# Kernel tuning notes

Hardware: AMD Instinct MI355X
Metric: run time of the kernel (lower is better)

## Reference

```python
import jax, jax.numpy as jnp
import numpy as np

DEPTH = 6
HEADS = 8
DIM = 512
DH = DIM // HEADS          # 64
SEQ = 512
BATCH = 8
MEM = 4096                 # KNN memory slots per batch element (scaled from 64000)
TOPK = 32                  # num_retrieved_memories
KNN_LAYERS = (3, 4)        # memorizing_layers=(4,5), 1-indexed -> 0-indexed 3,4
FF = 4 * DIM


def setup_inputs() -> dict:
    key = jax.random.key(0)
    ks = jax.random.split(key, 18)
    s = 0.02
    return {
        "x":     jax.random.normal(ks[0], (BATCH, SEQ, DIM), jnp.float32),
        "Wq":    jax.random.normal(ks[1], (DEPTH, DIM, DIM), jnp.float32) * s,
        "Wk":    jax.random.normal(ks[2], (DEPTH, DIM, DIM), jnp.float32) * s,
        "Wv":    jax.random.normal(ks[3], (DEPTH, DIM, DIM), jnp.float32) * s,
        "Wo":    jax.random.normal(ks[4], (DEPTH, DIM, DIM), jnp.float32) * s,
        "ln1_s": jnp.ones((DEPTH, DIM), jnp.float32),
        "ln1_b": jnp.zeros((DEPTH, DIM), jnp.float32),
        "ln2_s": jnp.ones((DEPTH, DIM), jnp.float32),
        "ln2_b": jnp.zeros((DEPTH, DIM), jnp.float32),
        "W1":    jax.random.normal(ks[5], (DEPTH, DIM, FF), jnp.float32) * s,
        "W2":    jax.random.normal(ks[6], (DEPTH, FF, DIM), jnp.float32) * s,
        "lnf_s": jnp.ones((DIM,), jnp.float32),
        "lnf_b": jnp.zeros((DIM,), jnp.float32),
        # pre-populated KNN memory banks (keys/values in head dim), one per memorizing layer
        "mem_k": jax.random.normal(ks[7], (len(KNN_LAYERS), BATCH, MEM, DH), jnp.float32),
        "mem_v": jax.random.normal(ks[8], (len(KNN_LAYERS), BATCH, MEM, DH), jnp.float32),
    }


def _ln(x, s, b):
    m = x.mean(-1, keepdims=True)
    v = ((x - m) ** 2).mean(-1, keepdims=True)
    return (x - m) * jax.lax.rsqrt(v + 1e-5) * s + b


def _gather_mem(mem, idx):
    # mem: (b, M, d), idx: (b, h, n, K) -> (b, h, n, K, d)
    return jax.vmap(lambda m, i: m[i])(mem, idx)


def reference(x, Wq, Wk, Wv, Wo, ln1_s, ln1_b, ln2_s, ln2_b, W1, W2,
              lnf_s, lnf_b, mem_k, mem_v):
    b, n, d = x.shape
    scale = DH ** -0.5
    causal = jnp.tril(jnp.ones((n, n), dtype=bool))
    neg = jnp.float32(-1e9)
    mem_i = 0
    for l in range(DEPTH):
        h = _ln(x, ln1_s[l], ln1_b[l])
        q = (h @ Wq[l]).reshape(b, n, HEADS, DH)
        k = (h @ Wk[l]).reshape(b, n, HEADS, DH)
        v = (h @ Wv[l]).reshape(b, n, HEADS, DH)
        sim = jnp.einsum('bihd,bjhd->bhij', q, k) * scale
        sim = jnp.where(causal, sim, neg)
        if l in KNN_LAYERS:
            mk, mv = mem_k[mem_i], mem_v[mem_i]              # (b, M, dh)
            # KNN search: dense scoring + top-k retrieval
            sim_all = jnp.einsum('bihd,bmd->bhim', q, mk) * scale  # (b,h,n,M)
            top_sim, top_idx = jax.lax.top_k(sim_all, TOPK)        # (b,h,n,K)
            gv = _gather_mem(mv, top_idx)                          # (b,h,n,K,dh)
            # joint softmax over [retrieved memories, local causal]
            logits = jnp.concatenate([top_sim, sim], axis=-1)
            attn = jax.nn.softmax(logits, axis=-1)
            a_mem, a_loc = attn[..., :TOPK], attn[..., TOPK:]
            out = (jnp.einsum('bhik,bhikd->bhid', a_mem, gv)
                   + jnp.einsum('bhij,bjhd->bhid', a_loc, v))
            mem_i += 1
        else:
            attn = jax.nn.softmax(sim, axis=-1)
            out = jnp.einsum('bhij,bjhd->bhid', attn, v)
        out = out.transpose(0, 2, 1, 3).reshape(b, n, d) @ Wo[l]
        x = x + out
        h2 = _ln(x, ln2_s[l], ln2_b[l])
        x = x + jax.nn.gelu(h2 @ W1[l]) @ W2[l]
    return _ln(x, lnf_s, lnf_b)
```

## Files before the change

kernel.cpp:

```cpp
#include <hip/hip_runtime.h>
#include <math.h>

#define BB 8
#define NN 512
#define DD 512
#define HH 8
#define DHH 64
#define FFF 2048
#define MEMM 4096
#define TOPKK 32
#define DEPTHH 6
#define NT (BB*NN)
#define QKVS 1536

typedef __bf16 bf16x8 __attribute__((ext_vector_type(8)));
typedef __bf16 bf16x4 __attribute__((ext_vector_type(4)));
typedef float f32x4 __attribute__((ext_vector_type(4)));

template <int OBF16>
__global__ __launch_bounds__(256) void ln_kernel(const float* __restrict__ xin,
                                                 const float* __restrict__ g,
                                                 const float* __restrict__ bt,
                                                 void* __restrict__ outv) {
  __shared__ float red[4];
  int tok = blockIdx.x;
  const float* xr = xin + (size_t)tok * DD;
  int t = threadIdx.x;
  float v0 = xr[t], v1 = xr[t + 256];
  float s = v0 + v1;
#pragma unroll
  for (int m = 32; m; m >>= 1) s += __shfl_xor(s, m, 64);
  if ((t & 63) == 0) red[t >> 6] = s;
  __syncthreads();
  float mean = (red[0] + red[1] + red[2] + red[3]) * (1.0f / 512.0f);
  float d0 = v0 - mean, d1 = v1 - mean;
  float vv = d0 * d0 + d1 * d1;
#pragma unroll
  for (int m = 32; m; m >>= 1) vv += __shfl_xor(vv, m, 64);
  __syncthreads();
  if ((t & 63) == 0) red[t >> 6] = vv;
  __syncthreads();
  float var = (red[0] + red[1] + red[2] + red[3]) * (1.0f / 512.0f);
  float inv = rsqrtf(var + 1e-5f);
  float o0 = d0 * inv * g[t] + bt[t];
  float o1 = d1 * inv * g[t + 256] + bt[t + 256];
  if (OBF16) {
    __bf16* out = (__bf16*)outv;
    out[(size_t)tok * DD + t] = (__bf16)o0;
    out[(size_t)tok * DD + t + 256] = (__bf16)o1;
  } else {
    float* out = (float*)outv;
    out[(size_t)tok * DD + t] = o0;
    out[(size_t)tok * DD + t + 256] = o1;
  }
}

__device__ inline float gelu_f(float x) {
  float x3 = x * x * x;
  return 0.5f * x * (1.0f + tanhf(0.7978845608028654f * (x + 0.044715f * x3)));
}

__global__ __launch_bounds__(256) void transpose_all_kernel(
    const float* __restrict__ Wq, const float* __restrict__ Wk,
    const float* __restrict__ Wv, const float* __restrict__ Wo,
    const float* __restrict__ W1, const float* __restrict__ W2,
    __bf16* __restrict__ wqT, __bf16* __restrict__ wkT,
    __bf16* __restrict__ wvT, __bf16* __restrict__ woT,
    __bf16* __restrict__ w1T, __bf16* __restrict__ w2T) {
  __shared__ float tile[32][33];
  int tid = blockIdx.x;
  const float* src; __bf16* dst; int K, N, tt;
  if (tid < 1024) {
    int which = tid >> 8; tt = tid & 255; K = 512; N = 512;
    src = (which == 0) ? Wq : (which == 1) ? Wk : (which == 2) ? Wv : Wo;
    dst = (which == 0) ? wqT : (which == 1) ? wkT : (which == 2) ? wvT : woT;
  } else if (tid < 2048) {
    tt = tid - 1024; K = 512; N = 2048; src = W1; dst = w1T;
  } else {
    tt = tid - 2048; K = 2048; N = 512; src = W2; dst = w2T;
  }
  int nx = N >> 5;
  int n0 = (tt % nx) * 32, k0 = (tt / nx) * 32;
  int tx = threadIdx.x & 31, ty = threadIdx.x >> 5;
#pragma unroll
  for (int i = 0; i < 4; i++) {
    int r = ty + i * 8;
    tile[r][tx] = src[(size_t)(k0 + r) * N + n0 + tx];
  }
  __syncthreads();
#pragma unroll
  for (int i = 0; i < 4; i++) {
    int r = ty + i * 8;
    dst[(size_t)(n0 + r) * K + k0 + tx] = (__bf16)tile[tx][r];
  }
}

__device__ __forceinline__ void gload16(const __bf16* g, __bf16* lds) {
  __builtin_amdgcn_global_load_lds(
      (const __attribute__((address_space(1))) void*)g,
      (__attribute__((address_space(3))) void*)lds, 16, 0, 0);
}

template <int EPI, int OBF16>
__global__ __launch_bounds__(256) void gemm_mfma128(const __bf16* __restrict__ A,
                                                    const __bf16* __restrict__ Bt,
                                                    const float* __restrict__ R,
                                                    void* __restrict__ Cout,
                                                    int M, int N, int K) {
  __shared__ __align__(16) __bf16 Als[128 * 64];
  __shared__ __align__(16) __bf16 Bls[128 * 64];
  int t = threadIdx.x;
  int bn = blockIdx.x, bm = blockIdx.y;
  int lane = t & 63, w = t >> 6;
  int wr = w >> 1, wc = w & 1;
  int m15 = lane & 15, q = lane >> 4;
  f32x4 acc[4][4] = {};
  for (int kt = 0; kt < K; kt += 64) {
    __syncthreads();
#pragma unroll
    for (int i = 0; i < 4; i++) {
      int rg = w * 32 + i * 8;
      int row = rg + (lane >> 3);
      int lcol = (lane & 7) * 8;
      gload16(A + (size_t)(bm * 128 + row) * K + kt + lcol, &Als[rg * 64]);
      gload16(Bt + (size_t)(bn * 128 + row) * K + kt + lcol, &Bls[rg * 64]);
    }
    __syncthreads();
#pragma unroll
    for (int ks = 0; ks < 2; ks++) {
      bf16x8 af[4], bfr[4];
#pragma unroll
      for (int mt = 0; mt < 4; mt++)
        af[mt] = *(const bf16x8*)&Als[(wr * 64 + mt * 16 + m15) * 64 + (ks * 4 + q) * 8];
#pragma unroll
      for (int nt = 0; nt < 4; nt++)
        bfr[nt] = *(const bf16x8*)&Bls[(wc * 64 + nt * 16 + m15) * 64 + (ks * 4 + q) * 8];
#pragma unroll
      for (int mt = 0; mt < 4; mt++)
#pragma unroll
        for (int nt = 0; nt < 4; nt++)
          acc[mt][nt] = __builtin_amdgcn_mfma_f32_16x16x32_bf16(af[mt], bfr[nt],
                                                                acc[mt][nt], 0, 0, 0);
    }
  }
#pragma unroll
  for (int mt = 0; mt < 4; mt++) {
#pragma unroll
    for (int nt = 0; nt < 4; nt++) {
      int gc = bn * 128 + wc * 64 + nt * 16 + m15;
#pragma unroll
      for (int r = 0; r < 4; r++) {
        int gr = bm * 128 + wr * 64 + mt * 16 + q * 4 + r;
        size_t off = (size_t)gr * N + gc;
        float v = acc[mt][nt][r];
        if (EPI == 1) v = gelu_f(v);
        if (EPI == 2) v += R[off];
        if (OBF16) ((__bf16*)Cout)[off] = (__bf16)v;
        else       ((float*)Cout)[off] = v;
      }
    }
  }
}

template <int EPI, int OBF16>
__global__ __launch_bounds__(256) void gemm_mfma64(const __bf16* __restrict__ A,
                                                   const __bf16* __restrict__ Bt,
                                                   const float* __restrict__ R,
                                                   void* __restrict__ Cout,
                                                   int M, int N, int K) {
  __shared__ __align__(16) __bf16 Als[128 * 64];
  __shared__ __align__(16) __bf16 Bls[64 * 64];
  int t = threadIdx.x;
  int bn = blockIdx.x, bm = blockIdx.y;
  int lane = t & 63, w = t >> 6;
  int wr = w >> 1, wc = w & 1;
  int m15 = lane & 15, q = lane >> 4;
  f32x4 acc[4][2] = {};
  for (int kt = 0; kt < K; kt += 64) {
    __syncthreads();
#pragma unroll
    for (int i = 0; i < 4; i++) {
      int rg = w * 32 + i * 8;
      int row = rg + (lane >> 3);
      int lcol = (lane & 7) * 8;
      gload16(A + (size_t)(bm * 128 + row) * K + kt + lcol, &Als[rg * 64]);
    }
#pragma unroll
    for (int i = 0; i < 2; i++) {
      int rg = w * 16 + i * 8;
      int row = rg + (lane >> 3);
      int lcol = (lane & 7) * 8;
      gload16(Bt + (size_t)(bn * 64 + row) * K + kt + lcol, &Bls[rg * 64]);
    }
    __syncthreads();
#pragma unroll
    for (int ks = 0; ks < 2; ks++) {
      bf16x8 af[4], bfr[2];
#pragma unroll
      for (int mt = 0; mt < 4; mt++)
        af[mt] = *(const bf16x8*)&Als[(wr * 64 + mt * 16 + m15) * 64 + (ks * 4 + q) * 8];
#pragma unroll
      for (int nt = 0; nt < 2; nt++)
        bfr[nt] = *(const bf16x8*)&Bls[(wc * 32 + nt * 16 + m15) * 64 + (ks * 4 + q) * 8];
#pragma unroll
      for (int mt = 0; mt < 4; mt++)
#pragma unroll
        for (int nt = 0; nt < 2; nt++)
          acc[mt][nt] = __builtin_amdgcn_mfma_f32_16x16x32_bf16(af[mt], bfr[nt],
                                                                acc[mt][nt], 0, 0, 0);
    }
  }
#pragma unroll
  for (int mt = 0; mt < 4; mt++) {
#pragma unroll
    for (int nt = 0; nt < 2; nt++) {
      int gc = bn * 64 + wc * 32 + nt * 16 + m15;
#pragma unroll
      for (int r = 0; r < 4; r++) {
        int gr = bm * 128 + wr * 64 + mt * 16 + q * 4 + r;
        size_t off = (size_t)gr * N + gc;
        float v = acc[mt][nt][r];
        if (EPI == 1) v = gelu_f(v);
        if (EPI == 2) v += R[off];
        if (OBF16) ((__bf16*)Cout)[off] = (__bf16)v;
        else       ((float*)Cout)[off] = v;
      }
    }
  }
}

__global__ __launch_bounds__(256) void split_bf16_kernel(const float* __restrict__ src,
                                                         __bf16* __restrict__ hi,
                                                         __bf16* __restrict__ lo) {
  int i = blockIdx.x * 256 + threadIdx.x;
  float4 v = ((const float4*)src)[i];
  float xs[4] = {v.x, v.y, v.z, v.w};
  bf16x4 hv, lv;
#pragma unroll
  for (int e = 0; e < 4; e++) {
    __bf16 h = (__bf16)xs[e];
    hv[e] = h;
    lv[e] = (__bf16)(xs[e] - (float)h);
  }
  *(bf16x4*)&hi[(size_t)i * 4] = hv;
  *(bf16x4*)&lo[(size_t)i * 4] = lv;
}

__global__ __launch_bounds__(256) void vtrans_split_kernel(const float* __restrict__ qkv,
                                                           __bf16* __restrict__ vth,
                                                           __bf16* __restrict__ vtl) {
  __shared__ float tile[64 * 68];
  int tt = blockIdx.x, h = blockIdx.y, b = blockIdx.z;
  int t = threadIdx.x;
#pragma unroll
  for (int i = 0; i < 4; i++) {
    int lin = i * 256 + t, row = lin >> 4, c = (lin & 15) * 4;
    float4 x = *(const float4*)(qkv + ((size_t)(b * NN) + tt * 64 + row) * QKVS + 1024 + h * DHH + c);
    *(float4*)&tile[row * 68 + c] = x;
  }
  __syncthreads();
  int d = t >> 2, tb = (t & 3) * 16;
  float xs[16];
#pragma unroll
  for (int j = 0; j < 16; j++) xs[j] = tile[(tb + j) * 68 + d];
  bf16x8 h0, h1, l0, l1;
#pragma unroll
  for (int j = 0; j < 8; j++) {
    __bf16 a = (__bf16)xs[j];
    h0[j] = a; l0[j] = (__bf16)(xs[j] - (float)a);
    __bf16 bmv = (__bf16)xs[8 + j];
    h1[j] = bmv; l1[j] = (__bf16)(xs[8 + j] - (float)bmv);
  }
  size_t ob = ((size_t)(b * HH + h) * 64 + d) * NN + tt * 64 + tb;
  *(bf16x8*)(vth + ob) = h0; *(bf16x8*)(vth + ob + 8) = h1;
  *(bf16x8*)(vtl + ob) = l0; *(bf16x8*)(vtl + ob + 8) = l1;
}

__global__ __launch_bounds__(256) void knn_score_mfma(const float* __restrict__ q,
                                                      const __bf16* __restrict__ khi,
                                                      const __bf16* __restrict__ klo,
                                                      float* __restrict__ S,
                                                      int bh0) {
  __shared__ __bf16 Kls[2][128 * 72];
  int it = blockIdx.x, bh = bh0 + blockIdx.y;
  int b = bh >> 3, h = bh & 7;
  int t = threadIdx.x;
  int lane = t & 63, w = t >> 6;
  int m15 = lane & 15, kg = lane >> 4;
  const float scale = 0.125f;

  bf16x8 aqh[2][2], aql[2][2];
#pragma unroll
  for (int rf = 0; rf < 2; rf++)
#pragma unroll
    for (int ks = 0; ks < 2; ks++) {
      const float* qp = q + ((size_t)(b * NN) + it * 32 + rf * 16 + m15) * QKVS +
                        h * DHH + ks * 32 + kg * 8;
      float4 x0 = *(const float4*)qp;
      float4 x1 = *(const float4*)(qp + 4);
      float xs[8] = {x0.x, x0.y, x0.z, x0.w, x1.x, x1.y, x1.z, x1.w};
#pragma unroll
      for (int e = 0; e < 8; e++) {
        __bf16 hv = (__bf16)xs[e];
        aqh[rf][ks][e] = hv;
        aql[rf][ks][e] = (__bf16)(xs[e] - (float)hv);
      }
    }

  const __bf16* khb = khi + (size_t)b * MEMM * DHH;
  const __bf16* klb = klo + (size_t)b * MEMM * DHH;
  size_t srow0 = (size_t)blockIdx.y * NN + it * 32;

  for (int mt = 0; mt < MEMM; mt += 128) {
    __syncthreads();
#pragma unroll
    for (int i = 0; i < 4; i++) {
      int lin = i * 256 + t;
      int row = lin >> 3, cb = (lin & 7) * 8;
      *(uint4*)&Kls[0][row * 72 + cb] = *(const uint4*)(khb + (size_t)(mt + row) * DHH + cb);
      *(uint4*)&Kls[1][row * 72 + cb] = *(const uint4*)(klb + (size_t)(mt + row) * DHH + cb);
    }
    __syncthreads();
    f32x4 acc[2][2] = {};
#pragma unroll
    for (int ks = 0; ks < 2; ks++) {
      bf16x8 bh2[2], bl2[2];
#pragma unroll
      for (int cf = 0; cf < 2; cf++) {
        int row = w * 32 + cf * 16 + m15;
        bh2[cf] = *(const bf16x8*)&Kls[0][row * 72 + ks * 32 + kg * 8];
        bl2[cf] = *(const bf16x8*)&Kls[1][row * 72 + ks * 32 + kg * 8];
      }
#pragma unroll
      for (int rf = 0; rf < 2; rf++)
#pragma unroll
        for (int cf = 0; cf < 2; cf++) {
          acc[rf][cf] = __builtin_amdgcn_mfma_f32_16x16x32_bf16(aqh[rf][ks], bh2[cf], acc[rf][cf], 0, 0, 0);
          acc[rf][cf] = __builtin_amdgcn_mfma_f32_16x16x32_bf16(aql[rf][ks], bh2[cf], acc[rf][cf], 0, 0, 0);
          acc[rf][cf] = __builtin_amdgcn_mfma_f32_16x16x32_bf16(aqh[rf][ks], bl2[cf], acc[rf][cf], 0, 0, 0);
        }
    }
#pragma unroll
    for (int rf = 0; rf < 2; rf++)
#pragma unroll
      for (int cf = 0; cf < 2; cf++) {
        int col = mt + w * 32 + cf * 16 + m15;
#pragma unroll
        for (int rr = 0; rr < 4; rr++)
          S[(srow0 + rf * 16 + kg * 4 + rr) * MEMM + col] = acc[rf][cf][rr] * scale;
      }
  }
}

__global__ __launch_bounds__(256, 4) void knn_select_kernel(const float* __restrict__ S,
                                                            float* __restrict__ topv,
                                                            int* __restrict__ topi,
                                                            int row_base) {
  int lane = threadIdx.x & 63;
  int row = blockIdx.x * 4 + (threadIdx.x >> 6);
  const float* srow = S + (size_t)row * MEMM;
  unsigned u[64];
#pragma unroll
  for (int i = 0; i < 64; i++) {
    union { float f; unsigned b; } cv;
    cv.f = srow[i * 64 + lane];
    unsigned b = cv.b;
    u[i] = (b & 0x80000000u) ? ~b : (b | 0x80000000u);
  }
  unsigned T = 0;
#pragma unroll 1
  for (int bit = 31; bit >= 0; --bit) {
    unsigned Tp = T | (1u << bit);
    int c = 0;
#pragma unroll
    for (int i = 0; i < 64; i++) c += (u[i] >= Tp) ? 1 : 0;
#pragma unroll
    for (int m = 32; m; m >>= 1) c += __shfl_xor(c, m, 64);
    if (c >= TOPKK) {
      T = Tp;
      if (c == TOPKK) break;
    }
  }
  unsigned long long below = (1ull << lane) - 1ull;
  float* tvrow = topv + (size_t)(row_base + row) * TOPKK;
  int* tirow = topi + (size_t)(row_base + row) * TOPKK;
  int g = 0;
#pragma unroll
  for (int i = 0; i < 64; i++) {
    bool f = u[i] > T;
    unsigned long long m = __ballot(f);
    if (f) {
      int pos = g + __popcll(m & below);
      union { unsigned b; float f2; } rv;
      rv.b = (u[i] & 0x80000000u) ? (u[i] & 0x7fffffffu) : ~u[i];
      tvrow[pos] = rv.f2;
      tirow[pos] = i * 64 + lane;
    }
    g += __popcll(m);
  }
#pragma unroll
  for (int i = 0; i < 64; i++) {
    if (g < TOPKK) {
      bool f = (u[i] == T);
      unsigned long long m = __ballot(f);
      if (f) {
        int pos = g + __popcll(m & below);
        if (pos < TOPKK) {
          union { unsigned b; float f2; } rv;
          rv.b = (T & 0x80000000u) ? (T & 0x7fffffffu) : ~T;
          tvrow[pos] = rv.f2;
          tirow[pos] = i * 64 + lane;
        }
      }
      g += __popcll(m);
    }
  }
}

__device__ __forceinline__ void insert32vi(float (&rtv)[32], int (&rti)[32],
                                           float sv, int idx, float& thr) {
  float mv = rtv[0], mv2 = INFINITY;
  int mi = 0;
#pragma unroll
  for (int k = 1; k < 32; k++) {
    float v = rtv[k];
    bool lt = v < mv;
    mv2 = lt ? mv : fminf(mv2, v);
    mv = lt ? v : mv;
    mi = lt ? k : mi;
  }
#pragma unroll
  for (int k = 0; k < 32; k++) {
    bool hit = (k == mi);
    rtv[k] = hit ? sv : rtv[k];
    rti[k] = hit ? idx : rti[k];
  }
  thr = fminf(mv2, sv);
}

__global__ __launch_bounds__(256) void knn_mfma_topk(const float* __restrict__ q,
                                                     const __bf16* __restrict__ khi,
                                                     const __bf16* __restrict__ klo,
                                                     float* __restrict__ topv,
                                                     int* __restrict__ topi) {
  __shared__ __bf16 Kls[2][128 * 72];
  __shared__ float scb[32][132];
  __shared__ unsigned short midx[32 * 260];
  __shared__ float rthr[8][32];
  int it = blockIdx.x, h = blockIdx.y, b = blockIdx.z;
  int t = threadIdx.x;
  int lane = t & 63, w = t >> 6;
  int m15 = lane & 15, kg = lane >> 4;
  const float scale = 0.125f;
  bf16x8 aqh[2][2], aql[2][2];
#pragma unroll
  for (int rf = 0; rf < 2; rf++)
#pragma unroll
    for (int ks = 0; ks < 2; ks++) {
      const float* qp = q + ((size_t)(b * NN) + it * 32 + rf * 16 + m15) * QKVS +
                        h * DHH + ks * 32 + kg * 8;
      float4 x0 = *(const float4*)qp;
      float4 x1 = *(const float4*)(qp + 4);
      float xs[8] = {x0.x, x0.y, x0.z, x0.w, x1.x, x1.y, x1.z, x1.w};
#pragma unroll
      for (int e = 0; e < 8; e++) {
        __bf16 hv = (__bf16)xs[e];
        aqh[rf][ks][e] = hv;
        aql[rf][ks][e] = (__bf16)(xs[e] - (float)hv);
      }
    }
  int r = t & 31, p = t >> 5;
  rthr[p][r] = -INFINITY;
  float rtv[32]; int rti[32];
#pragma unroll
  for (int k = 0; k < 32; k++) { rtv[k] = -INFINITY; rti[k] = 0; }
  float thr = -INFINITY;
  const __bf16* khb = khi + (size_t)b * MEMM * DHH;
  const __bf16* klb = klo + (size_t)b * MEMM * DHH;

  for (int mt = 0; mt < MEMM; mt += 128) {
    __syncthreads();
#pragma unroll
    for (int i = 0; i < 4; i++) {
      int lin = i * 256 + t;
      int row = lin >> 3, cb = (lin & 7) * 8;
      *(uint4*)&Kls[0][row * 72 + cb] = *(const uint4*)(khb + (size_t)(mt + row) * DHH + cb);
      *(uint4*)&Kls[1][row * 72 + cb] = *(const uint4*)(klb + (size_t)(mt + row) * DHH + cb);
    }
    __syncthreads();
    f32x4 acc[2][2] = {};
#pragma unroll
    for (int ks = 0; ks < 2; ks++) {
      bf16x8 bh2[2], bl2[2];
#pragma unroll
      for (int cf = 0; cf < 2; cf++) {
        int row = w * 32 + cf * 16 + m15;
        bh2[cf] = *(const bf16x8*)&Kls[0][row * 72 + ks * 32 + kg * 8];
        bl2[cf] = *(const bf16x8*)&Kls[1][row * 72 + ks * 32 + kg * 8];
      }
#pragma unroll
      for (int rf = 0; rf < 2; rf++)
#pragma unroll
        for (int cf = 0; cf < 2; cf++) {
          acc[rf][cf] = __builtin_amdgcn_mfma_f32_16x16x32_bf16(aqh[rf][ks], bh2[cf], acc[rf][cf], 0, 0, 0);
          acc[rf][cf] = __builtin_amdgcn_mfma_f32_16x16x32_bf16(aql[rf][ks], bh2[cf], acc[rf][cf], 0, 0, 0);
          acc[rf][cf] = __builtin_amdgcn_mfma_f32_16x16x32_bf16(aqh[rf][ks], bl2[cf], acc[rf][cf], 0, 0, 0);
        }
    }
#pragma unroll
    for (int rf = 0; rf < 2; rf++)
#pragma unroll
      for (int cf = 0; cf < 2; cf++) {
        int col = w * 32 + cf * 16 + m15;
#pragma unroll
        for (int rr = 0; rr < 4; rr++)
          scb[rf * 16 + kg * 4 + rr][col] = acc[rf][cf][rr] * scale;
      }
    __syncthreads();
    {
      float B2 = rthr[0][r];
#pragma unroll
      for (int j = 1; j < 8; j++) B2 = fmaxf(B2, rthr[j][r]);
      const float* srow = &scb[r][16 * p];
#pragma unroll 1
      for (int c = 0; c < 16; c++) {
        int cc = (c + r) & 15;
        float sv = srow[cc];
        if (sv > fmaxf(thr, B2))
          insert32vi(rtv, rti, sv, mt + 16 * p + cc, thr);
      }
      rthr[p][r] = thr;
    }
  }
  __syncthreads();
  float* mvals = (float*)&Kls[0][0];
#pragma unroll
  for (int k = 0; k < 32; k++) {
    int cc = (k + r) & 31;
    mvals[(size_t)260 * r + 32 * p + cc] = rtv[k];
    midx[(size_t)260 * r + 32 * p + cc] = (unsigned short)rti[k];
  }
  __syncthreads();
  if (t < 32) {
#pragma unroll 1
    for (int c = 0; c < 224; c++) {
      int cc = c + r; if (cc >= 224) cc -= 224;
      float sv = mvals[(size_t)260 * r + 32 + cc];
      if (sv > thr)
        insert32vi(rtv, rti, sv, (int)midx[(size_t)260 * r + 32 + cc], thr);
    }
    size_t rowg = ((size_t)b * HH + h) * NN + it * 32 + r;
#pragma unroll
    for (int k = 0; k < 32; k++) {
      topv[rowg * TOPKK + k] = rtv[k];
      topi[rowg * TOPKK + k] = rti[k];
    }
  }
}

__global__ __launch_bounds__(256) void attn_mfma_kernel(
    const float* __restrict__ qkv,
    const __bf16* __restrict__ vth, const __bf16* __restrict__ vtl,
    __bf16* __restrict__ ao, const float* __restrict__ topv,
    const int* __restrict__ topi, const float* __restrict__ mem_v, int knn) {
  __shared__ __align__(16) __bf16 smem[27648];
  __bf16* Kh = smem;
  __bf16* Kl = smem + 4608;
  __bf16* Vh = smem + 9216;
  __bf16* Vl = smem + 13824;
  __bf16* Pw = smem + 18432;

  int flat = blockIdx.x;
  int bi = flat >> 6;
  int hb = flat & 63;
  int h = hb & 7, b = hb >> 3;
  int t = threadIdx.x, lane = t & 63, w = t >> 6;
  int q15 = lane & 15, g = lane >> 4;
  const float scale = 0.125f;

  bf16x8 qh[2], ql[2];
  {
    const float* qp = qkv + ((size_t)(b * NN) + bi * 64 + w * 16 + q15) * QKVS + h * DHH;
#pragma unroll
    for (int ks = 0; ks < 2; ks++) {
      float4 x0 = *(const float4*)(qp + ks * 32 + g * 8);
      float4 x1 = *(const float4*)(qp + ks * 32 + g * 8 + 4);
      float xs[8] = {x0.x, x0.y, x0.z, x0.w, x1.x, x1.y, x1.z, x1.w};
#pragma unroll
      for (int e = 0; e < 8; e++) {
        __bf16 hv = (__bf16)xs[e];
        qh[ks][e] = hv;
        ql[ks][e] = (__bf16)(xs[e] - (float)hv);
      }
    }
  }
  int tr = t >> 4, kc = (t & 15) * 4;
  int td = t >> 3, tb = (t & 7) * 8;
  float4 kp0, kp1, kp2, kp3;
  uint4 vhp0, vhp1, vlp0, vlp1;

#define LOAD_TILE(jt_) do {                                                        \
    const float* kb_ = qkv + ((size_t)(b * NN) + (jt_) * 64 + tr) * QKVS + 512 +   \
                       h * DHH + kc;                                               \
    kp0 = *(const float4*)kb_;                                                     \
    kp1 = *(const float4*)(kb_ + (size_t)16 * QKVS);                               \
    kp2 = *(const float4*)(kb_ + (size_t)32 * QKVS);                               \
    kp3 = *(const float4*)(kb_ + (size_t)48 * QKVS);                               \
    size_t vb_ = ((size_t)(b * HH + h) * 64 + td) * NN + (jt_) * 64 + tb;          \
    vhp0 = *(const uint4*)(vth + vb_);                                             \
    vhp1 = *(const uint4*)(vth + vb_ + (size_t)32 * NN);                           \
    vlp0 = *(const uint4*)(vtl + vb_);                                             \
    vlp1 = *(const uint4*)(vtl + vb_ + (size_t)32 * NN);                           \
  } while (0)

#define STORE_K(kp_, ro_) do {                                                     \
    bf16x4 hv_, lv_;                                                               \
    float e0_ = kp_.x, e1_ = kp_.y, e2_ = kp_.z, e3_ = kp_.w;                      \
    hv_[0] = (__bf16)e0_; lv_[0] = (__bf16)(e0_ - (float)hv_[0]);                  \
    hv_[1] = (__bf16)e1_; lv_[1] = (__bf16)(e1_ - (float)hv_[1]);                  \
    hv_[2] = (__bf16)e2_; lv_[2] = (__bf16)(e2_ - (float)hv_[2]);                  \
    hv_[3] = (__bf16)e3_; lv_[3] = (__bf16)(e3_ - (float)hv_[3]);                  \
    *(bf16x4*)&Kh[((ro_) + tr) * 72 + kc] = hv_;                                   \
    *(bf16x4*)&Kl[((ro_) + tr) * 72 + kc] = lv_;                                   \
  } while (0)

  float m_run = -INFINITY, l_run = 0.f;
  f32x4 opv[4] = {};
  int ntiles = bi + 1;
  LOAD_TILE(0);
  for (int jt = 0; jt < ntiles; jt++) {
    __syncthreads();
    STORE_K(kp0, 0); STORE_K(kp1, 16); STORE_K(kp2, 32); STORE_K(kp3, 48);
    *(uint4*)&Vh[td * 72 + tb] = vhp0;
    *(uint4*)&Vh[(32 + td) * 72 + tb] = vhp1;
    *(uint4*)&Vl[td * 72 + tb] = vlp0;
    *(uint4*)&Vl[(32 + td) * 72 + tb] = vlp1;
    if (jt + 1 < ntiles) LOAD_TILE(jt + 1);
    __syncthreads();
    int smax = (jt == bi) ? w : 3;
    float sc16[16];
    float tmax = -INFINITY;
#pragma unroll
    for (int s = 0; s < 4; s++) {
      if (s <= smax) {
        f32x4 accs = {};
#pragma unroll
        for (int ks = 0; ks < 2; ks++) {
          bf16x8 ah = *(const bf16x8*)&Kh[(s * 16 + q15) * 72 + ks * 32 + g * 8];
          bf16x8 al = *(const bf16x8*)&Kl[(s * 16 + q15) * 72 + ks * 32 + g * 8];
          accs = __builtin_amdgcn_mfma_f32_16x16x32_bf16(ah, qh[ks], accs, 0, 0, 0);
          accs = __builtin_amdgcn_mfma_f32_16x16x32_bf16(al, qh[ks], accs, 0, 0, 0);
          accs = __builtin_amdgcn_mfma_f32_16x16x32_bf16(ah, ql[ks], accs, 0, 0, 0);
        }
#pragma unroll
        for (int r = 0; r < 4; r++) {
          float sv = accs[r] * scale;
          if (jt == bi) {
            int kvg = jt * 64 + s * 16 + g * 4 + r;
            int qg = bi * 64 + w * 16 + q15;
            if (kvg > qg) sv = -INFINITY;
          }
          sc16[s * 4 + r] = sv;
          tmax = fmaxf(tmax, sv);
        }
      } else {
#pragma unroll
        for (int r = 0; r < 4; r++) sc16[s * 4 + r] = -INFINITY;
      }
    }
    tmax = fmaxf(tmax, __shfl_xor(tmax, 16, 64));
    tmax = fmaxf(tmax, __shfl_xor(tmax, 32, 64));
    float m_new = fmaxf(m_run, tmax);
    float psum = 0.f;
    __bf16 ph[16], pl[16];
#pragma unroll
    for (int i = 0; i < 16; i++) {
      float p = __expf(sc16[i] - m_new);
      psum += p;
      __bf16 hp = (__bf16)p;
      ph[i] = hp; pl[i] = (__bf16)(p - (float)hp);
    }
    psum += __shfl_xor(psum, 16, 64);
    psum += __shfl_xor(psum, 32, 64);
    float alpha = __expf(m_run - m_new);
    l_run = l_run * alpha + psum;
    m_run = m_new;
    __bf16* Ph = Pw + (w * 2 + 0) * 1152;
    __bf16* Pl = Pw + (w * 2 + 1) * 1152;
#pragma unroll
    for (int s = 0; s < 4; s++) {
      bf16x4 hv, lv;
#pragma unroll
      for (int r = 0; r < 4; r++) { hv[r] = ph[s * 4 + r]; lv[r] = pl[s * 4 + r]; }
      *(bf16x4*)&Ph[q15 * 72 + s * 16 + g * 4] = hv;
      *(bf16x4*)&Pl[q15 * 72 + s * 16 + g * 4] = lv;
    }
    __builtin_amdgcn_wave_barrier();
    float a0 = __shfl(alpha, g * 4 + 0, 64);
    float a1 = __shfl(alpha, g * 4 + 1, 64);
    float a2 = __shfl(alpha, g * 4 + 2, 64);
    float a3 = __shfl(alpha, g * 4 + 3, 64);
#pragma unroll
    for (int dsub = 0; dsub < 4; dsub++) {
      opv[dsub][0] *= a0; opv[dsub][1] *= a1;
      opv[dsub][2] *= a2; opv[dsub][3] *= a3;
    }
#pragma unroll
    for (int ks2 = 0; ks2 < 2; ks2++) {
      bf16x8 pah = *(const bf16x8*)&Ph[q15 * 72 + ks2 * 32 + g * 8];
      bf16x8 pal = *(const bf16x8*)&Pl[q15 * 72 + ks2 * 32 + g * 8];
#pragma unroll
      for (int dsub = 0; dsub < 4; dsub++) {
        bf16x8 vbh = *(const bf16x8*)&Vh[(dsub * 16 + q15) * 72 + ks2 * 32 + g * 8];
        bf16x8 vbl = *(const bf16x8*)&Vl[(dsub * 16 + q15) * 72 + ks2 * 32 + g * 8];
        opv[dsub] = __builtin_amdgcn_mfma_f32_16x16x32_bf16(pah, vbh, opv[dsub], 0, 0, 0);
        opv[dsub] = __builtin_amdgcn_mfma_f32_16x16x32_bf16(pal, vbh, opv[dsub], 0, 0, 0);
        opv[dsub] = __builtin_amdgcn_mfma_f32_16x16x32_bf16(pah, vbl, opv[dsub], 0, 0, 0);
      }
    }
  }
#undef LOAD_TILE
#undef STORE_K
  __syncthreads();
  float* scf  = (float*)smem;
  float* marr = (float*)(smem + 8704);
  float* larr = marr + 64;
  float* aarr = marr + 128;
  float* sc2  = (float*)(smem + 9216);
  int*   pidx = (int*)(smem + 13824);
#pragma unroll
  for (int dsub = 0; dsub < 4; dsub++)
#pragma unroll
    for (int r = 0; r < 4; r++)
      scf[(w * 16 + g * 4 + r) * 68 + dsub * 16 + q15] = opv[dsub][r];
  if (g == 0) { marr[w * 16 + q15] = m_run; larr[w * 16 + q15] = l_run; }
  __syncthreads();
  int r_ = t & 63, w4 = t >> 6;
  float acc16[16];
  if (knn) {
    size_t rowbase = ((size_t)b * HH + h) * NN + bi * 64;
    for (int rr = w * 16; rr < w * 16 + 16; rr++) {
      float s = (lane < TOPKK) ? topv[(rowbase + rr) * TOPKK + lane] : -INFINITY;
      float m_old = marr[rr];
      float tm = s;
#pragma unroll
      for (int m = 32; m; m >>= 1) tm = fmaxf(tm, __shfl_xor(tm, m, 64));
      float m_new = fmaxf(m_old, tm);
      float p = __expf(s - m_new);
      float ts = p;
#pragma unroll
      for (int m = 32; m; m >>= 1) ts += __shfl_xor(ts, m, 64);
      float alpha = __expf(m_old - m_new);
      if (lane < TOPKK) {
        sc2[rr * 33 + lane] = p;
        pidx[rr * 32 + lane] = topi[(rowbase + rr) * TOPKK + lane];
      }
      if (lane == 0) {
        marr[rr] = m_new; larr[rr] = larr[rr] * alpha + ts; aarr[rr] = alpha;
      }
    }
    __syncthreads();
    float al = aarr[r_];
#pragma unroll
    for (int dd = 0; dd < 16; dd++) acc16[dd] = scf[r_ * 68 + w4 * 16 + dd] * al;
    const float* mvb = mem_v + (size_t)b * MEMM * DHH;
#pragma unroll 1
    for (int kk = 0; kk < TOPKK; kk++) {
      float p = sc2[r_ * 33 + kk];
      const float* mrow = mvb + (size_t)pidx[r_ * 32 + kk] * DHH + w4 * 16;
#pragma unroll
      for (int dd = 0; dd < 16; dd += 4) {
        float4 m4 = *(const float4*)(mrow + dd);
        acc16[dd] += p * m4.x; acc16[dd + 1] += p * m4.y;
        acc16[dd + 2] += p * m4.z; acc16[dd + 3] += p * m4.w;
      }
    }
  } else {
#pragma unroll
    for (int dd = 0; dd < 16; dd++) acc16[dd] = scf[r_ * 68 + w4 * 16 + dd];
  }
  float linv = 1.f / larr[r_];
  bf16x8 o0, o1;
#pragma unroll
  for (int j = 0; j < 8; j++) {
    o0[j] = (__bf16)(acc16[j] * linv);
    o1[j] = (__bf16)(acc16[8 + j] * linv);
  }
  __bf16* aop = ao + ((size_t)(b * NN) + bi * 64 + r_) * DD + h * DHH + w4 * 16;
  *(bf16x8*)aop = o0;
  *(bf16x8*)(aop + 8) = o1;
}

extern "C" void kernel_launch(void* const* d_in, const int* in_sizes, int n_in,
                              void* d_out, int out_size, void* d_ws, size_t ws_size,
                              hipStream_t stream) {
  const float* x_in  = (const float*)d_in[0];
  const float* Wq    = (const float*)d_in[1];
  const float* Wk    = (const float*)d_in[2];
  const float* Wv    = (const float*)d_in[3];
  const float* Wo    = (const float*)d_in[4];
  const float* ln1_s = (const float*)d_in[5];
  const float* ln1_b = (const float*)d_in[6];
  const float* ln2_s = (const float*)d_in[7];
  const float* ln2_b = (const float*)d_in[8];
  const float* W1    = (const float*)d_in[9];
  const float* W2    = (const float*)d_in[10];
  const float* lnf_s = (const float*)d_in[11];
  const float* lnf_b = (const float*)d_in[12];
  const float* mem_k = (const float*)d_in[13];
  const float* mem_v = (const float*)d_in[14];

  float* ws  = (float*)d_ws;
  float*  xb    = ws;
  float*  qkvb  = ws + 2097152;
  __bf16* hb16  = (__bf16*)(ws + 8388608);
  __bf16* ao16  = (__bf16*)(ws + 9437184);
  __bf16* wqT   = (__bf16*)(ws + 10485760);
  __bf16* woT   = (__bf16*)(ws + 10878976);
  __bf16* w1T   = (__bf16*)(ws + 11010048);
  __bf16* w2T   = (__bf16*)(ws + 11534336);
  float*  tvb   = ws + 12058624;
  int*    tib   = (int*)(ws + 13107200);
  __bf16* ffb16 = (__bf16*)(ws + 2097152);
  __bf16* wkT   = wqT + 262144;
  __bf16* wvT   = wqT + 524288;
  __bf16* khi16 = (__bf16*)(ws + 8388608);
  __bf16* klo16 = (__bf16*)(ws + 9437184);

  const size_t base_floats = 14155776;
  const size_t slice_floats = (size_t)NN * MEMM;
  const size_t ws_floats = ws_size / sizeof(float);
  int nbh = 0;
  for (int c = 16; c >= 1; c >>= 1) {
    if (base_floats + (size_t)c * slice_floats <= ws_floats) { nbh = c; break; }
  }
  float* Sb = ws + base_floats;
  __bf16* vth = (__bf16*)(ws + base_floats);
  __bf16* vtl = (__bf16*)(ws + base_floats + 1048576);

  dim3 blk(256);
  const size_t DD2 = (size_t)DD * DD;
  for (int l = 0; l < DEPTHH; l++) {
    const float* xcur = (l == 0) ? x_in : xb;
    transpose_all_kernel<<<dim3(3072), blk, 0, stream>>>(
        Wq + l * DD2, Wk + l * DD2, Wv + l * DD2, Wo + l * DD2,
        W1 + (size_t)l * DD * FFF, W2 + (size_t)l * FFF * DD,
        wqT, wkT, wvT, woT, w1T, w2T);

    ln_kernel<1><<<NT, blk, 0, stream>>>(xcur, ln1_s + l * DD, ln1_b + l * DD, hb16);
    gemm_mfma64<0, 0><<<dim3(24, 32), blk, 0, stream>>>(hb16, wqT, nullptr, qkvb, NT, QKVS, DD);
    int mi = (l == 3) ? 0 : ((l == 4) ? 1 : -1);
    if (mi >= 0) {
      const float* mk = mem_k + (size_t)mi * BB * MEMM * DHH;
      split_bf16_kernel<<<dim3(BB * MEMM * DHH / 1024), blk, 0, stream>>>(mk, khi16, klo16);
      if (nbh > 0) {
        for (int bh0 = 0; bh0 < BB * HH; bh0 += nbh) {
          knn_score_mfma<<<dim3(16, nbh), blk, 0, stream>>>(qkvb, khi16, klo16, Sb, bh0);
          knn_select_kernel<<<dim3(nbh * NN / 4), blk, 0, stream>>>(Sb, tvb, tib, bh0 * NN);
        }
      } else {
        knn_mfma_topk<<<dim3(16, 8, 8), blk, 0, stream>>>(qkvb, khi16, klo16, tvb, tib);
      }
    }
    vtrans_split_kernel<<<dim3(8, 8, 8), blk, 0, stream>>>(qkvb, vth, vtl);
    attn_mfma_kernel<<<dim3(512), blk, 0, stream>>>(
        qkvb, vth, vtl, ao16, tvb, tib,
        mem_v + (size_t)(mi < 0 ? 0 : mi) * BB * MEMM * DHH, mi >= 0 ? 1 : 0);
    gemm_mfma64<2, 0><<<dim3(8, 32), blk, 0, stream>>>(ao16, woT, xcur, xb, NT, DD, DD);
    ln_kernel<1><<<NT, blk, 0, stream>>>(xb, ln2_s + l * DD, ln2_b + l * DD, hb16);
    gemm_mfma128<1, 1><<<dim3(16, 32), blk, 0, stream>>>(hb16, w1T, nullptr, ffb16, NT, FFF, DD);
    gemm_mfma64<2, 0><<<dim3(8, 32), blk, 0, stream>>>(ffb16, w2T, xb, xb, NT, DD, FFF);
  }
  ln_kernel<0><<<NT, blk, 0, stream>>>(xb, lnf_s, lnf_b, (float*)d_out);
}
```

Baseline: 1.910 ms.

## Enlarge KNN score tile, vectorize top-k select loads, allow larger score batches

The KNN scoring kernel now computes 64 query rows per block instead of 32, so each K tile staged in LDS is reused by twice as many MFMAs, and the grid shrinks to 8 row-tiles. The select kernel loads scores as uint4 per lane rather than strided scalars, and remaps output indices to match the new element order. The tie-fill loop now exits early once 32 entries are found. The host may also batch up to 64 (b,h) pairs per score/select launch when the workspace allows, which cuts launch count but needs more scratch and raises register pressure in the score kernel.

```diff
diff --git a/kernel.cpp b/kernel.cpp
--- a/kernel.cpp
+++ b/kernel.cpp
@@ -289,12 +289,12 @@
   int m15 = lane & 15, kg = lane >> 4;
   const float scale = 0.125f;
 
-  bf16x8 aqh[2][2], aql[2][2];
-#pragma unroll
-  for (int rf = 0; rf < 2; rf++)
+  bf16x8 aqh[4][2], aql[4][2];
+#pragma unroll
+  for (int rf = 0; rf < 4; rf++)
 #pragma unroll
     for (int ks = 0; ks < 2; ks++) {
-      const float* qp = q + ((size_t)(b * NN) + it * 32 + rf * 16 + m15) * QKVS +
+      const float* qp = q + ((size_t)(b * NN) + it * 64 + rf * 16 + m15) * QKVS +
                         h * DHH + ks * 32 + kg * 8;
       float4 x0 = *(const float4*)qp;
       float4 x1 = *(const float4*)(qp + 4);
@@ -309,7 +309,7 @@
 
   const __bf16* khb = khi + (size_t)b * MEMM * DHH;
   const __bf16* klb = klo + (size_t)b * MEMM * DHH;
-  size_t srow0 = (size_t)blockIdx.y * NN + it * 32;
+  size_t srow0 = (size_t)blockIdx.y * NN + it * 64;
 
   for (int mt = 0; mt < MEMM; mt += 128) {
     __syncthreads();
@@ -321,7 +321,7 @@
       *(uint4*)&Kls[1][row * 72 + cb] = *(const uint4*)(klb + (size_t)(mt + row) * DHH + cb);
     }
     __syncthreads();
-    f32x4 acc[2][2] = {};
+    f32x4 acc[4][2] = {};
 #pragma unroll
     for (int ks = 0; ks < 2; ks++) {
       bf16x8 bh2[2], bl2[2];
@@ -332,7 +332,7 @@
         bl2[cf] = *(const bf16x8*)&Kls[1][row * 72 + ks * 32 + kg * 8];
       }
 #pragma unroll
-      for (int rf = 0; rf < 2; rf++)
+      for (int rf = 0; rf < 4; rf++)
 #pragma unroll
         for (int cf = 0; cf < 2; cf++) {
           acc[rf][cf] = __builtin_amdgcn_mfma_f32_16x16x32_bf16(aqh[rf][ks], bh2[cf], acc[rf][cf], 0, 0, 0);
@@ -341,7 +341,7 @@
         }
     }
 #pragma unroll
-    for (int rf = 0; rf < 2; rf++)
+    for (int rf = 0; rf < 4; rf++)
 #pragma unroll
       for (int cf = 0; cf < 2; cf++) {
         int col = mt + w * 32 + cf * 16 + m15;
@@ -361,11 +361,14 @@
   const float* srow = S + (size_t)row * MEMM;
   unsigned u[64];
 #pragma unroll
-  for (int i = 0; i < 64; i++) {
-    union { float f; unsigned b; } cv;
-    cv.f = srow[i * 64 + lane];
-    unsigned b = cv.b;
-    u[i] = (b & 0x80000000u) ? ~b : (b | 0x80000000u);
+  for (int i = 0; i < 16; i++) {
+    uint4 v = *(const uint4*)(srow + i * 256 + lane * 4);
+    unsigned vs[4] = {v.x, v.y, v.z, v.w};
+#pragma unroll
+    for (int e = 0; e < 4; e++) {
+      unsigned bb = vs[e];
+      u[i * 4 + e] = (bb & 0x80000000u) ? ~bb : (bb | 0x80000000u);
+    }
   }
   unsigned T = 0;
 #pragma unroll 1
@@ -373,7 +376,7 @@
     unsigned Tp = T | (1u << bit);
     int c = 0;
 #pragma unroll
-    for (int i = 0; i < 64; i++) c += (u[i] >= Tp) ? 1 : 0;
+    for (int j = 0; j < 64; j++) c += (u[j] >= Tp) ? 1 : 0;
 #pragma unroll
     for (int m = 32; m; m >>= 1) c += __shfl_xor(c, m, 64);
     if (c >= TOPKK) {
@@ -386,22 +389,27 @@
   int* tirow = topi + (size_t)(row_base + row) * TOPKK;
   int g = 0;
 #pragma unroll
-  for (int i = 0; i < 64; i++) {
-    bool f = u[i] > T;
-    unsigned long long m = __ballot(f);
-    if (f) {
-      int pos = g + __popcll(m & below);
-      union { unsigned b; float f2; } rv;
-      rv.b = (u[i] & 0x80000000u) ? (u[i] & 0x7fffffffu) : ~u[i];
-      tvrow[pos] = rv.f2;
-      tirow[pos] = i * 64 + lane;
-    }
-    g += __popcll(m);
-  }
-#pragma unroll
-  for (int i = 0; i < 64; i++) {
-    if (g < TOPKK) {
-      bool f = (u[i] == T);
+  for (int i = 0; i < 16; i++)
+#pragma unroll
+    for (int e = 0; e < 4; e++) {
+      int j = i * 4 + e;
+      bool f = u[j] > T;
+      unsigned long long m = __ballot(f);
+      if (f) {
+        int pos = g + __popcll(m & below);
+        union { unsigned b; float f2; } rv;
+        rv.b = (u[j] & 0x80000000u) ? (u[j] & 0x7fffffffu) : ~u[j];
+        tvrow[pos] = rv.f2;
+        tirow[pos] = i * 256 + lane * 4 + e;
+      }
+      g += __popcll(m);
+    }
+#pragma unroll 1
+  for (int i = 0; i < 16 && g < TOPKK; i++)
+#pragma unroll
+    for (int e = 0; e < 4; e++) {
+      int j = i * 4 + e;
+      bool f = (u[j] == T);
       unsigned long long m = __ballot(f);
       if (f) {
         int pos = g + __popcll(m & below);
@@ -409,12 +417,11 @@
           union { unsigned b; float f2; } rv;
           rv.b = (T & 0x80000000u) ? (T & 0x7fffffffu) : ~T;
           tvrow[pos] = rv.f2;
-          tirow[pos] = i * 64 + lane;
+          tirow[pos] = i * 256 + lane * 4 + e;
         }
       }
       g += __popcll(m);
     }
-  }
 }
 
 __device__ __forceinline__ void insert32vi(float (&rtv)[32], int (&rti)[32],
@@ -831,7 +838,7 @@
   const size_t slice_floats = (size_t)NN * MEMM;
   const size_t ws_floats = ws_size / sizeof(float);
   int nbh = 0;
-  for (int c = 16; c >= 1; c >>= 1) {
+  for (int c = 64; c >= 1; c >>= 1) {
     if (base_floats + (size_t)c * slice_floats <= ws_floats) { nbh = c; break; }
   }
   float* Sb = ws + base_floats;
@@ -855,7 +862,7 @@
       split_bf16_kernel<<<dim3(BB * MEMM * DHH / 1024), blk, 0, stream>>>(mk, khi16, klo16);
       if (nbh > 0) {
         for (int bh0 = 0; bh0 < BB * HH; bh0 += nbh) {
-          knn_score_mfma<<<dim3(16, nbh), blk, 0, stream>>>(qkvb, khi16, klo16, Sb, bh0);
+          knn_score_mfma<<<dim3(8, nbh), blk, 0, stream>>>(qkvb, khi16, klo16, Sb, bh0);
           knn_select_kernel<<<dim3(nbh * NN / 4), blk, 0, stream>>>(Sb, tvb, tib, bh0 * NN);
         }
       } else {
```

After: 2.131 ms. 1.12x slower.
